# Optimization experiments

Measured on AMD Instinct MI355X. Metric: run time of the kernel, lower is better.

The kernel has to match this reference:

```python
import jax, jax.numpy as jnp
import numpy as np

D_MODEL = 1024
EXPAND = 2
D_INNER = D_MODEL * EXPAND  # 2048
D_STATE = 16
D_CONV = 4
DT_RANK = (D_MODEL + 15) // 16  # 64
BATCH = 2
SEQ = 1024


def setup_inputs() -> dict:
    key = jax.random.key(0)
    ks = jax.random.split(key, 10)
    s = lambda d: 1.0 / np.sqrt(d)
    x = jax.random.normal(ks[0], (BATCH, SEQ, D_MODEL), dtype=jnp.float32)
    W_in = jax.random.normal(ks[1], (D_MODEL, 2 * D_INNER), dtype=jnp.float32) * s(D_MODEL)
    conv_w = jax.random.normal(ks[2], (D_INNER, D_CONV), dtype=jnp.float32) * s(D_CONV)
    conv_b = jax.random.normal(ks[3], (D_INNER,), dtype=jnp.float32) * 0.02
    W_x = jax.random.normal(ks[4], (D_INNER, DT_RANK + 2 * D_STATE), dtype=jnp.float32) * s(D_INNER)
    W_dt = jax.random.normal(ks[5], (DT_RANK, D_INNER), dtype=jnp.float32) * s(DT_RANK)
    b_dt = jax.random.uniform(ks[6], (D_INNER,), dtype=jnp.float32, minval=-4.0, maxval=-2.0)
    # S4D-real init: A = -[1..d_state] per channel
    A_log = jnp.log(jnp.tile(jnp.arange(1, D_STATE + 1, dtype=jnp.float32), (D_INNER, 1)))
    D = jnp.ones((D_INNER,), dtype=jnp.float32)
    W_out = jax.random.normal(ks[7], (D_INNER, D_MODEL), dtype=jnp.float32) * s(D_INNER)
    return {"x": x, "W_in": W_in, "conv_w": conv_w, "conv_b": conv_b,
            "W_x": W_x, "W_dt": W_dt, "b_dt": b_dt, "A_log": A_log,
            "D": D, "W_out": W_out}


def _mamba_forward(x, W_in, conv_w, conv_b, W_x, W_dt, b_dt, A_log, D, W_out):
    B, L, _ = x.shape
    # input projection -> [B, L, 2*d_inner], split into u (conv branch) and z (gate)
    xz = jnp.einsum('bld,de->ble', x, W_in)
    u, z = jnp.split(xz, 2, axis=-1)  # each [B, L, d_inner]

    # causal depthwise conv over time
    u_c = jnp.transpose(u, (0, 2, 1))                      # [B, d_inner, L]
    u_c = jnp.pad(u_c, ((0, 0), (0, 0), (D_CONV - 1, 0)))  # left pad for causality
    kern = conv_w[:, None, :]                              # [d_inner, 1, d_conv]
    u_c = jax.lax.conv_general_dilated(
        u_c, kern, window_strides=(1,), padding='VALID',
        dimension_numbers=('NCH', 'OIH', 'NCH'),
        feature_group_count=D_INNER)
    u_c = u_c + conv_b[None, :, None]
    u_c = jax.nn.silu(jnp.transpose(u_c, (0, 2, 1)))       # [B, L, d_inner]

    # data-dependent SSM parameters
    x_dbl = jnp.einsum('bld,de->ble', u_c, W_x)            # [B, L, dt_rank+2*d_state]
    dt_lowrank = x_dbl[..., :DT_RANK]
    Bmat = x_dbl[..., DT_RANK:DT_RANK + D_STATE]           # [B, L, d_state]
    Cmat = x_dbl[..., DT_RANK + D_STATE:]                  # [B, L, d_state]
    dt = jax.nn.softplus(jnp.einsum('blr,rd->bld', dt_lowrank, W_dt) + b_dt)

    A = -jnp.exp(A_log)                                    # [d_inner, d_state]

    # selective scan over time: h' = exp(dt*A) h + dt*B*u ; y = <h, C>
    def step(h, inp):
        u_t, dt_t, B_t, C_t = inp                          # [B,d], [B,d], [B,n], [B,n]
        dA = jnp.exp(dt_t[..., None] * A)                  # [B, d_inner, d_state]
        dBu = (dt_t * u_t)[..., None] * B_t[:, None, :]    # [B, d_inner, d_state]
        h = dA * h + dBu
        y_t = jnp.einsum('bdn,bn->bd', h, C_t)
        return h, y_t

    h0 = jnp.zeros((B, D_INNER, D_STATE), dtype=x.dtype)
    seq = (jnp.swapaxes(u_c, 0, 1), jnp.swapaxes(dt, 0, 1),
           jnp.swapaxes(Bmat, 0, 1), jnp.swapaxes(Cmat, 0, 1))
    _, ys = jax.lax.scan(step, h0, seq)                    # ys: [L, B, d_inner]
    y = jnp.swapaxes(ys, 0, 1) + u_c * D                   # skip term
    y = y * jax.nn.silu(z)                                 # gate
    return jnp.einsum('bld,de->ble', y, W_out)             # [B, L, d_model]


def reference(x, W_in, conv_w, conv_b, W_x, W_dt, b_dt, A_log, D, W_out):
    return _mamba_forward(x, W_in, conv_w, conv_b, W_x, W_dt, b_dt, A_log, D, W_out)
```

## Files before the change

kernel.cpp:

```cpp
#include <hip/hip_runtime.h>
#include <hip/hip_bf16.h>


typedef __attribute__((ext_vector_type(8))) short bfrag;
typedef __attribute__((ext_vector_type(4))) float f32x4;

#define CF   32
#define CLEN 32

__device__ __forceinline__ unsigned short f2bf(float f) {
    unsigned int u = __float_as_uint(f);
    u += 0x7FFF + ((u >> 16) & 1);
    return (unsigned short)(u >> 16);
}
__device__ __forceinline__ float bf2f(unsigned short s) {
    return __uint_as_float((unsigned int)s << 16);
}

template<int MT>
__global__ __launch_bounds__(256) void gemm_bf16(
    const unsigned short* __restrict__ A,
    const unsigned short* __restrict__ BT,
    float* __restrict__ C,
    unsigned short* __restrict__ C1,
    int K, int lda, int ldb, int ldc, int split)
{
    constexpr int FJ = (MT == 128) ? 4 : 2;
    __shared__ unsigned short sA[MT][40];
    __shared__ unsigned short sB[128][40];

    const int tid  = threadIdx.x;
    const int wave = tid >> 6, lane = tid & 63;
    const int lm   = lane & 15;
    const int quad = lane >> 4;
    const int kb   = quad << 3;
    const int wrow = (MT == 128) ? ((wave >> 1) << 6) : 0;
    const int wcol = (MT == 128) ? ((wave & 1) << 6) : (wave << 5);
    const int bm = blockIdx.y * MT, bn = blockIdx.x * 128;

    const int srow = tid >> 2;
    const int scol = (tid & 3) << 3;

    f32x4 acc[4][FJ];
    #pragma unroll
    for (int i = 0; i < 4; ++i)
        #pragma unroll
        for (int j = 0; j < FJ; ++j) {
            acc[i][j][0] = 0.f; acc[i][j][1] = 0.f;
            acc[i][j][2] = 0.f; acc[i][j][3] = 0.f;
        }

    for (int k0 = 0; k0 < K; k0 += 32) {
        *(float4*)&sA[srow][scol] = *(const float4*)&A[(size_t)(bm + srow) * lda + k0 + scol];
        if (MT == 128)
            *(float4*)&sA[srow + 64][scol] = *(const float4*)&A[(size_t)(bm + srow + 64) * lda + k0 + scol];
        *(float4*)&sB[srow][scol]      = *(const float4*)&BT[(size_t)(bn + srow)      * ldb + k0 + scol];
        *(float4*)&sB[srow + 64][scol] = *(const float4*)&BT[(size_t)(bn + srow + 64) * ldb + k0 + scol];
        __syncthreads();

        bfrag af[4], bf[FJ];
        #pragma unroll
        for (int i = 0; i < 4; ++i) af[i] = *(const bfrag*)&sA[wrow + i * 16 + lm][kb];
        #pragma unroll
        for (int j = 0; j < FJ; ++j) bf[j] = *(const bfrag*)&sB[wcol + j * 16 + lm][kb];

        #pragma unroll
        for (int i = 0; i < 4; ++i)
            #pragma unroll
            for (int j = 0; j < FJ; ++j)
                acc[i][j] = __builtin_amdgcn_mfma_f32_16x16x32_bf16(
                    af[i], bf[j], acc[i][j], 0, 0, 0);
        __syncthreads();
    }

    #pragma unroll
    for (int i = 0; i < 4; ++i)
        #pragma unroll
        for (int j = 0; j < FJ; ++j) {
            const int col = bn + wcol + j * 16 + lm;
            #pragma unroll
            for (int r = 0; r < 4; ++r) {
                const int row = bm + wrow + i * 16 + quad * 4 + r;
                float v = acc[i][j][r];
                if (split > 0) {
                    if (col < split) C [(size_t)row * split + col] = v;
                    else             C1[(size_t)row * split + (col - split)] = f2bf(v);
                } else {
                    C[(size_t)row * ldc + col] = v;
                }
            }
        }
}

__global__ __launch_bounds__(256) void transpose_cast(
    const float* __restrict__ in, unsigned short* __restrict__ out,
    int rows, int cols)
{
    __shared__ float tile[32][33];
    const int j0 = blockIdx.x * 32, i0 = blockIdx.y * 32;
    const int tx = threadIdx.x & 31, ty = threadIdx.x >> 5;
    #pragma unroll
    for (int k = 0; k < 4; ++k)
        tile[ty + 8 * k][tx] = in[(size_t)(i0 + ty + 8 * k) * cols + j0 + tx];
    __syncthreads();
    #pragma unroll
    for (int k = 0; k < 4; ++k)
        out[(size_t)(j0 + ty + 8 * k) * rows + i0 + tx] = f2bf(tile[tx][ty + 8 * k]);
}

__global__ __launch_bounds__(256) void cast_bf16(
    const float* __restrict__ in, unsigned short* __restrict__ out)
{
    int i = (blockIdx.x * 256 + threadIdx.x) * 4;
    float4 v = *(const float4*)&in[i];
    ushort4 o;
    o.x = f2bf(v.x); o.y = f2bf(v.y); o.z = f2bf(v.z); o.w = f2bf(v.w);
    *(ushort4*)&out[i] = o;
}

#define SK_KS 128
__global__ __launch_bounds__(256) void gemm_f32_splitk(
    const float* __restrict__ A, const float* __restrict__ B,
    float* __restrict__ part)
{
    __shared__ __align__(16) float As[16][64];
    __shared__ __align__(16) float Bs[16][96];

    const int tid = threadIdx.x;
    const int mtile = blockIdx.x >> 4;
    const int kslice = blockIdx.x & 15;
    const int bm = mtile * 64;
    const int kbase = kslice * SK_KS;

    const int am = tid >> 2;
    const int ak = (tid & 3) << 2;

    const int ty = tid >> 4, tx = tid & 15;
    const int rm = ty << 2;
    const int rn = tx * 6;

    float acc[4][6] = {};

    for (int k0 = 0; k0 < SK_KS; k0 += 16) {
        float4 av = *(const float4*)&A[(size_t)(bm + am) * 2048 + kbase + k0 + ak];
        As[ak + 0][am] = av.x;
        As[ak + 1][am] = av.y;
        As[ak + 2][am] = av.z;
        As[ak + 3][am] = av.w;
        for (int i = tid; i < 384; i += 256) {
            int br = i / 24, bc = (i % 24) << 2;
            *(float4*)&Bs[br][bc] = *(const float4*)&B[(size_t)(kbase + k0 + br) * 96 + bc];
        }
        __syncthreads();

        #pragma unroll
        for (int k = 0; k < 16; ++k) {
            float4 a = *(const float4*)&As[k][rm];
            float b[6];
            #pragma unroll
            for (int j = 0; j < 6; ++j) b[j] = Bs[k][rn + j];
            #pragma unroll
            for (int j = 0; j < 6; ++j) {
                acc[0][j] += a.x * b[j];
                acc[1][j] += a.y * b[j];
                acc[2][j] += a.z * b[j];
                acc[3][j] += a.w * b[j];
            }
        }
        __syncthreads();
    }

    float* pout = part + (size_t)kslice * 196608;
    #pragma unroll
    for (int i = 0; i < 4; ++i) {
        float* crow = pout + (size_t)(bm + rm + i) * 96 + rn;
        #pragma unroll
        for (int j = 0; j < 6; ++j)
            crow[j] = acc[i][j];
    }
}

__global__ __launch_bounds__(256) void reduce_splitk(
    const float* __restrict__ part, float* __restrict__ xdbl)
{
    int i = (blockIdx.x * 256 + threadIdx.x) * 4;
    float4 acc = {0.f, 0.f, 0.f, 0.f};
    #pragma unroll
    for (int s = 0; s < 16; ++s) {
        float4 v = *(const float4*)&part[(size_t)s * 196608 + i];
        acc.x += v.x; acc.y += v.y; acc.z += v.z; acc.w += v.w;
    }
    *(float4*)&xdbl[i] = acc;
}

#define BM 64
#define BN 64
#define BK 16
__global__ __launch_bounds__(256) void gemm_f32(
    const float* __restrict__ A, const float* __restrict__ B,
    float* __restrict__ C, int M, int N, int K,
    int lda, int ldb, int ldc, int mode, const float* __restrict__ bias)
{
    __shared__ __align__(16) float As[BK][BM];
    __shared__ __align__(16) float Bs[BK][BN];

    const int tid = threadIdx.x;
    const int bm = blockIdx.y * BM;
    const int bn = blockIdx.x * BN;

    const int am = tid >> 2;
    const int ak = (tid & 3) << 2;
    const int bk = tid >> 4;
    const int bnn = (tid & 15) << 2;

    const int tx = tid & 15, ty = tid >> 4;
    const int rm = ty << 2;
    const int rn = tx << 2;
    const int cm = bm + rm, cn = bn + rn;

    float acc[4][4] = {};

    for (int k0 = 0; k0 < K; k0 += BK) {
        const float* ap = A + (size_t)(bm + am) * lda + (k0 + ak);
        float4 av = *(const float4*)ap;
        As[ak + 0][am] = av.x;
        As[ak + 1][am] = av.y;
        As[ak + 2][am] = av.z;
        As[ak + 3][am] = av.w;
        {
            const int ncol = bn + bnn;
            const float* bp = B + (size_t)(k0 + bk) * ldb + ncol;
            float4 bv;
            if (ncol + 3 < N) {
                bv = *(const float4*)bp;
            } else {
                bv.x = (ncol + 0 < N) ? bp[0] : 0.f;
                bv.y = (ncol + 1 < N) ? bp[1] : 0.f;
                bv.z = (ncol + 2 < N) ? bp[2] : 0.f;
                bv.w = (ncol + 3 < N) ? bp[3] : 0.f;
            }
            *(float4*)&Bs[bk][bnn] = bv;
        }
        __syncthreads();

        #pragma unroll
        for (int k = 0; k < BK; ++k) {
            float4 a = *(const float4*)&As[k][rm];
            float4 b = *(const float4*)&Bs[k][rn];
            acc[0][0] += a.x * b.x; acc[0][1] += a.x * b.y;
            acc[0][2] += a.x * b.z; acc[0][3] += a.x * b.w;
            acc[1][0] += a.y * b.x; acc[1][1] += a.y * b.y;
            acc[1][2] += a.y * b.z; acc[1][3] += a.y * b.w;
            acc[2][0] += a.z * b.x; acc[2][1] += a.z * b.y;
            acc[2][2] += a.z * b.z; acc[2][3] += a.z * b.w;
            acc[3][0] += a.w * b.x; acc[3][1] += a.w * b.y;
            acc[3][2] += a.w * b.z; acc[3][3] += a.w * b.w;
        }
        __syncthreads();
    }

    #pragma unroll
    for (int i = 0; i < 4; ++i) {
        float* crow = C + (size_t)(cm + i) * ldc;
        #pragma unroll
        for (int j = 0; j < 4; ++j) {
            int col = cn + j;
            if (col < N) {
                float v = acc[i][j];
                if (mode == 1) {
                    v += bias[col];
                    v = (v > 20.f) ? v : logf(1.f + expf(v));
                }
                crow[col] = v;
            }
        }
    }
}

__global__ __launch_bounds__(256) void conv_silu_kernel(
    const float* __restrict__ upre, const float* __restrict__ cw,
    const float* __restrict__ cb, float* __restrict__ uc)
{
    int idx = blockIdx.x * 256 + threadIdx.x;
    int d = idx & 2047;
    int r = idx >> 11;
    int l = r & 1023;

    float4 w4 = *(const float4*)(cw + 4 * d);
    float w[4] = { w4.x, w4.y, w4.z, w4.w };
    float acc = cb[d];
    const float* up = upre + (size_t)r * 2048 + d;
    if (l >= 3) {
        acc += w[0] * up[-3 * 2048] + w[1] * up[-2 * 2048]
             + w[2] * up[-1 * 2048] + w[3] * up[0];
    } else {
        #pragma unroll
        for (int j = 0; j < 4; ++j) {
            int lj = l - 3 + j;
            if (lj >= 0) acc += w[j] * up[(j - 3) * 2048];
        }
    }
    float sig = 1.f / (1.f + expf(-acc));
    uc[idx] = acc * sig;
}

__global__ __launch_bounds__(256) void scan_pass1(
    const float* __restrict__ uc,
    const float* __restrict__ dtb,
    const float* __restrict__ xdbl,
    const float* __restrict__ A_log,
    float* __restrict__ Hend,
    float* __restrict__ Sdt)
{
    __shared__ float sB[CLEN][16];
    const int tid = threadIdx.x;
    const int bx  = blockIdx.x;
    const int c   = bx & (CF - 1);
    const int g   = (bx >> 5) & 7;
    const int b   = bx >> 8;
    const int d   = g * 256 + tid;
    const size_t rowbase = (size_t)b * 1024 + c * CLEN;

    for (int i = tid; i < CLEN * 16; i += 256) {
        int tt = i >> 4, nn = i & 15;
        sB[tt][nn] = xdbl[(rowbase + tt) * 96 + 64 + nn];
    }

    float A2[16];
    {
        float al[16];
        #pragma unroll
        for (int q = 0; q < 4; ++q)
            *(float4*)&al[4 * q] = *(const float4*)&A_log[(size_t)d * 16 + 4 * q];
        #pragma unroll
        for (int n = 0; n < 16; ++n) A2[n] = -expf(al[n]) * 1.44269504f;
    }
    __syncthreads();

    float h[16];
    #pragma unroll
    for (int n = 0; n < 16; ++n) h[n] = 0.f;
    float sdt = 0.f;

    #pragma unroll 4
    for (int t = 0; t < CLEN; ++t) {
        size_t r = rowbase + t;
        float dtv = dtb[r * 2048 + d];
        float uv  = uc [r * 2048 + d];
        sdt += dtv;
        float dtu = dtv * uv;
        float bl[16];
        #pragma unroll
        for (int q = 0; q < 4; ++q)
            *(float4*)&bl[4 * q] = *(const float4*)&sB[t][4 * q];
        #pragma unroll
        for (int n = 0; n < 16; ++n)
            h[n] = exp2f(dtv * A2[n]) * h[n] + dtu * bl[n];
    }

    size_t base = ((size_t)(b * CF + c) * 2048 + d) * 16;
    #pragma unroll
    for (int q = 0; q < 4; ++q)
        *(float4*)&Hend[base + 4 * q] = *(float4*)&h[4 * q];
    Sdt[(size_t)(b * CF + c) * 2048 + d] = sdt;
}

__global__ __launch_bounds__(256) void scan_pass2(
    const float* __restrict__ Hend, const float* __restrict__ Sdt,
    const float* __restrict__ A_log, float* __restrict__ Hin)
{
    int gid = blockIdx.x * 256 + threadIdx.x;
    int b = gid >> 15;
    int rest = gid & 32767;
    int d = rest >> 4;
    float A2 = -expf(A_log[rest]) * 1.44269504f;
    float H = 0.f;
    #pragma unroll
    for (int c = 0; c < CF; ++c) {
        size_t sidx = (size_t)(b * CF + c) * 2048 + d;
        size_t idx  = ((size_t)(b * CF + c) << 15) + rest;
        Hin[idx] = H;
        H = exp2f(A2 * Sdt[sidx]) * H + Hend[idx];
    }
}

__global__ __launch_bounds__(256) void scan_pass3(
    const float* __restrict__ uc,
    const float* __restrict__ dtb,
    const unsigned short* __restrict__ zb,
    const float* __restrict__ xdbl,
    const float* __restrict__ A_log,
    const float* __restrict__ Dvec,
    const float* __restrict__ Hin,
    unsigned short* __restrict__ yb)
{
    __shared__ float sBC[CLEN][32];
    const int tid = threadIdx.x;
    const int bx  = blockIdx.x;
    const int c   = bx & (CF - 1);
    const int g   = (bx >> 5) & 7;
    const int b   = bx >> 8;
    const int d   = g * 256 + tid;
    const size_t rowbase = (size_t)b * 1024 + c * CLEN;

    for (int i = tid; i < CLEN * 32; i += 256) {
        int tt = i >> 5, j = i & 31;
        sBC[tt][j] = xdbl[(rowbase + tt) * 96 + 64 + j];
    }

    float A2[16];
    {
        float al[16];
        #pragma unroll
        for (int q = 0; q < 4; ++q)
            *(float4*)&al[4 * q] = *(const float4*)&A_log[(size_t)d * 16 + 4 * q];
        #pragma unroll
        for (int n = 0; n < 16; ++n) A2[n] = -expf(al[n]) * 1.44269504f;
    }
    const float Dd = Dvec[d];

    float h[16];
    {
        size_t base = ((size_t)(b * CF + c) * 2048 + d) * 16;
        #pragma unroll
        for (int q = 0; q < 4; ++q)
            *(float4*)&h[4 * q] = *(const float4*)&Hin[base + 4 * q];
    }
    __syncthreads();

    #pragma unroll 2
    for (int t = 0; t < CLEN; ++t) {
        size_t r = rowbase + t;
        float dtv = dtb[r * 2048 + d];
        float uv  = uc [r * 2048 + d];
        float zv  = bf2f(zb[r * 2048 + d]);
        float dtu = dtv * uv;
        float bl[16], cl[16];
        #pragma unroll
        for (int q = 0; q < 4; ++q) {
            *(float4*)&bl[4 * q] = *(const float4*)&sBC[t][4 * q];
            *(float4*)&cl[4 * q] = *(const float4*)&sBC[t][16 + 4 * q];
        }
        float acc = uv * Dd;
        #pragma unroll
        for (int n = 0; n < 16; ++n) {
            h[n] = exp2f(dtv * A2[n]) * h[n] + dtu * bl[n];
            acc += h[n] * cl[n];
        }
        float yv = acc * zv / (1.f + expf(-zv));
        yb[r * 2048 + d] = f2bf(yv);
    }
}

extern "C" void kernel_launch(void* const* d_in, const int* in_sizes, int n_in,
                              void* d_out, int out_size, void* d_ws, size_t ws_size,
                              hipStream_t stream)
{
    const float* x      = (const float*)d_in[0];
    const float* W_in   = (const float*)d_in[1];
    const float* conv_w = (const float*)d_in[2];
    const float* conv_b = (const float*)d_in[3];
    const float* W_x    = (const float*)d_in[4];
    const float* W_dt   = (const float*)d_in[5];
    const float* b_dt   = (const float*)d_in[6];
    const float* A_log  = (const float*)d_in[7];
    const float* Dv     = (const float*)d_in[8];
    const float* W_out  = (const float*)d_in[9];
    float* out = (float*)d_out;

    float* ws    = (float*)d_ws;
    float* upre  = ws;
    float* dtb   = upre;
    float* uc    = ws + 4194304;
    float* xdbl  = uc + 4194304;
    float* Hend  = xdbl + 196608;
    float* Hin   = Hend + 2097152;
    float* Sdt   = Hin + 2097152;
    float* part  = Hend;
    unsigned short* zb   = (unsigned short*)(Sdt + 131072);
    unsigned short* xb   = zb + 4194304;
    unsigned short* wbT  = xb + 2097152;
    unsigned short* wobT = wbT + 4194304;
    unsigned short* yb   = wbT;

    dim3 blk(256);

    transpose_cast<<<dim3(128, 32), blk, 0, stream>>>(W_in, wbT, 1024, 4096);
    transpose_cast<<<dim3(32, 64), blk, 0, stream>>>(W_out, wobT, 2048, 1024);
    cast_bf16<<<2048, blk, 0, stream>>>(x, xb);

    gemm_bf16<128><<<dim3(32, 16), blk, 0, stream>>>(
        xb, wbT, upre, zb, 1024, 1024, 1024, 0, 2048);

    conv_silu_kernel<<<(2048 * 2048) / 256, blk, 0, stream>>>(upre, conv_w, conv_b, uc);

    gemm_f32_splitk<<<512, blk, 0, stream>>>(uc, W_x, part);
    reduce_splitk<<<192, blk, 0, stream>>>(part, xdbl);

    gemm_f32<<<dim3(32, 32), blk, 0, stream>>>(
        xdbl, W_dt, dtb, 2048, 2048, 64, 96, 2048, 2048, 1, b_dt);

    scan_pass1<<<512, blk, 0, stream>>>(uc, dtb, xdbl, A_log, Hend, Sdt);
    scan_pass2<<<256, blk, 0, stream>>>(Hend, Sdt, A_log, Hin);
    scan_pass3<<<512, blk, 0, stream>>>(uc, dtb, zb, xdbl, A_log, Dv, Hin, yb);

    gemm_bf16<64><<<dim3(8, 32), blk, 0, stream>>>(
        yb, wobT, out, nullptr, 2048, 2048, 2048, 1024, 0);
}
```

Before: 296.1 us.

## Use direct global-to-LDS async loads with XOR-swizzled tiles in bf16 GEMMs

Rewrites the bf16 MFMA GEMM so tiles go straight from global memory into LDS through global_load_lds instead of passing through registers. The K step grows from 32 to 64 and the LDS layout uses an XOR swizzle to avoid bank conflicts. The 64-row variant now uses a 2x2 wave layout. There is still one buffer and a barrier each iteration, so load and compute do not overlap, and the swizzle indexing relies on global_load_lds writing per-lane contiguous 16-byte slots.

Measured after the change: 281.2 us. 1.05x faster.

```diff
diff --git a/kernel.cpp b/kernel.cpp
--- a/kernel.cpp
+++ b/kernel.cpp
@@ -17,66 +17,92 @@
     return __uint_as_float((unsigned int)s << 16);
 }
 
+__device__ __forceinline__ void async_copy16(const unsigned short* g,
+                                             unsigned short* l) {
+    __builtin_amdgcn_global_load_lds(
+        (const __attribute__((address_space(1))) void*)g,
+        (__attribute__((address_space(3))) void*)l, 16, 0, 0);
+}
+
 template<int MT>
-__global__ __launch_bounds__(256) void gemm_bf16(
+__global__ __launch_bounds__(256) void gemm_bf16_v2(
     const unsigned short* __restrict__ A,
     const unsigned short* __restrict__ BT,
     float* __restrict__ C,
     unsigned short* __restrict__ C1,
     int K, int lda, int ldb, int ldc, int split)
 {
-    constexpr int FJ = (MT == 128) ? 4 : 2;
-    __shared__ unsigned short sA[MT][40];
-    __shared__ unsigned short sB[128][40];
+    constexpr int FI  = MT / 32;
+    constexpr int ACH = MT / 32;
+    __shared__ __align__(16) unsigned short sA[MT * 64];
+    __shared__ __align__(16) unsigned short sB[128 * 64];
 
     const int tid  = threadIdx.x;
     const int wave = tid >> 6, lane = tid & 63;
     const int lm   = lane & 15;
     const int quad = lane >> 4;
-    const int kb   = quad << 3;
-    const int wrow = (MT == 128) ? ((wave >> 1) << 6) : 0;
-    const int wcol = (MT == 128) ? ((wave & 1) << 6) : (wave << 5);
+    const int wrow = (wave >> 1) * (MT / 2);
+    const int wcol = (wave & 1) * 64;
     const int bm = blockIdx.y * MT, bn = blockIdx.x * 128;
 
-    const int srow = tid >> 2;
-    const int scol = (tid & 3) << 3;
-
-    f32x4 acc[4][FJ];
-    #pragma unroll
-    for (int i = 0; i < 4; ++i)
-        #pragma unroll
-        for (int j = 0; j < FJ; ++j) {
+    const int lrow = lane >> 3;
+    const int lkb  = (lane & 7) ^ lrow;
+
+    f32x4 acc[FI][4];
+    #pragma unroll
+    for (int i = 0; i < FI; ++i)
+        #pragma unroll
+        for (int j = 0; j < 4; ++j) {
             acc[i][j][0] = 0.f; acc[i][j][1] = 0.f;
             acc[i][j][2] = 0.f; acc[i][j][3] = 0.f;
         }
 
-    for (int k0 = 0; k0 < K; k0 += 32) {
-        *(float4*)&sA[srow][scol] = *(const float4*)&A[(size_t)(bm + srow) * lda + k0 + scol];
-        if (MT == 128)
-            *(float4*)&sA[srow + 64][scol] = *(const float4*)&A[(size_t)(bm + srow + 64) * lda + k0 + scol];
-        *(float4*)&sB[srow][scol]      = *(const float4*)&BT[(size_t)(bn + srow)      * ldb + k0 + scol];
-        *(float4*)&sB[srow + 64][scol] = *(const float4*)&BT[(size_t)(bn + srow + 64) * ldb + k0 + scol];
+    for (int k0 = 0; k0 < K; k0 += 64) {
+        #pragma unroll
+        for (int c = 0; c < ACH; ++c) {
+            const int chunk = wave * ACH + c;
+            const int row = chunk * 8 + lrow;
+            async_copy16(&A[(size_t)(bm + row) * lda + k0 + lkb * 8],
+                         &sA[chunk * 512 + lane * 8]);
+        }
+        #pragma unroll
+        for (int c = 0; c < 4; ++c) {
+            const int chunk = wave * 4 + c;
+            const int row = chunk * 8 + lrow;
+            async_copy16(&BT[(size_t)(bn + row) * ldb + k0 + lkb * 8],
+                         &sB[chunk * 512 + lane * 8]);
+        }
         __syncthreads();
 
-        bfrag af[4], bf[FJ];
-        #pragma unroll
-        for (int i = 0; i < 4; ++i) af[i] = *(const bfrag*)&sA[wrow + i * 16 + lm][kb];
-        #pragma unroll
-        for (int j = 0; j < FJ; ++j) bf[j] = *(const bfrag*)&sB[wcol + j * 16 + lm][kb];
-
-        #pragma unroll
-        for (int i = 0; i < 4; ++i)
+        #pragma unroll
+        for (int ks = 0; ks < 2; ++ks) {
+            bfrag af[FI], bf[4];
             #pragma unroll
-            for (int j = 0; j < FJ; ++j)
-                acc[i][j] = __builtin_amdgcn_mfma_f32_16x16x32_bf16(
-                    af[i], bf[j], acc[i][j], 0, 0, 0);
+            for (int i = 0; i < FI; ++i) {
+                const int row = wrow + i * 16 + lm;
+                const int slot = (ks * 4 + quad) ^ (row & 7);
+                af[i] = *(const bfrag*)&sA[row * 64 + slot * 8];
+            }
+            #pragma unroll
+            for (int j = 0; j < 4; ++j) {
+                const int row = wcol + j * 16 + lm;
+                const int slot = (ks * 4 + quad) ^ (row & 7);
+                bf[j] = *(const bfrag*)&sB[row * 64 + slot * 8];
+            }
+            #pragma unroll
+            for (int i = 0; i < FI; ++i)
+                #pragma unroll
+                for (int j = 0; j < 4; ++j)
+                    acc[i][j] = __builtin_amdgcn_mfma_f32_16x16x32_bf16(
+                        af[i], bf[j], acc[i][j], 0, 0, 0);
+        }
         __syncthreads();
     }
 
     #pragma unroll
-    for (int i = 0; i < 4; ++i)
-        #pragma unroll
-        for (int j = 0; j < FJ; ++j) {
+    for (int i = 0; i < FI; ++i)
+        #pragma unroll
+        for (int j = 0; j < 4; ++j) {
             const int col = bn + wcol + j * 16 + lm;
             #pragma unroll
             for (int r = 0; r < 4; ++r) {
@@ -489,7 +515,7 @@
     transpose_cast<<<dim3(32, 64), blk, 0, stream>>>(W_out, wobT, 2048, 1024);
     cast_bf16<<<2048, blk, 0, stream>>>(x, xb);
 
-    gemm_bf16<128><<<dim3(32, 16), blk, 0, stream>>>(
+    gemm_bf16_v2<128><<<dim3(32, 16), blk, 0, stream>>>(
         xb, wbT, upre, zb, 1024, 1024, 1024, 0, 2048);
 
     conv_silu_kernel<<<(2048 * 2048) / 256, blk, 0, stream>>>(upre, conv_w, conv_b, uc);
@@ -504,6 +530,6 @@
     scan_pass2<<<256, blk, 0, stream>>>(Hend, Sdt, A_log, Hin);
     scan_pass3<<<512, blk, 0, stream>>>(uc, dtb, zb, xdbl, A_log, Dv, Hin, yb);
 
-    gemm_bf16<64><<<dim3(8, 32), blk, 0, stream>>>(
+    gemm_bf16_v2<64><<<dim3(8, 32), blk, 0, stream>>>(
         yb, wobT, out, nullptr, 2048, 2048, 2048, 1024, 0);
 }
```
